# Optimization experiments

Measured on AMD Instinct MI355X. Metric: run time of the kernel, lower is better.

## Reference

```python
import jax, jax.numpy as jnp
import numpy as np

K = 3  # number_layers

def setup_inputs() -> dict:
    key = jax.random.key(0)
    k1, k2, k3, k4 = jax.random.split(key, 4)
    N, F_in, F_out, E, D = 100000, 256, 64, 1600000, 8
    x = jax.random.normal(k1, (N, F_in), dtype=jnp.float32)
    edge_attr = jax.random.uniform(k2, (E, D), dtype=jnp.float32)
    W = jax.random.normal(k3, (F_in, F_out), dtype=jnp.float32) / np.sqrt(F_in)
    b = jnp.zeros((F_out,), dtype=jnp.float32)
    edge_index = jax.random.randint(k4, (2, E), 0, N, dtype=jnp.int64)
    return {"x": x, "edge_attr": edge_attr, "W": W, "b": b, "edge_index": edge_index}

def reference(x, edge_attr, W, b, edge_index):
    N = x.shape[0]
    # edge_weight from edge_attr
    w = edge_attr.mean(axis=1)  # [E]
    src, dst = edge_index[0], edge_index[1]
    # gcn_norm: add self-loops with weight 1, symmetric normalization
    loop = jnp.arange(N, dtype=edge_index.dtype)
    src_f = jnp.concatenate([src, loop])
    dst_f = jnp.concatenate([dst, loop])
    w_f = jnp.concatenate([w, jnp.ones((N,), dtype=x.dtype)])
    deg = jax.ops.segment_sum(w_f, dst_f, num_segments=N)  # in-degree
    dinv = jnp.where(deg > 0, jax.lax.rsqrt(deg), 0.0)
    norm = dinv[src_f] * w_f * dinv[dst_f]  # [E+N]
    # K hops of x <- A_hat x
    h = x
    for _ in range(K):
        msg = norm[:, None] * h[src_f]              # gather [E+N, F]
        h = jax.ops.segment_sum(msg, dst_f, num_segments=N)  # scatter-add
    out = h @ W + b
    out = jax.nn.relu(out)
    # dropout is a no-op in eval mode
    return jax.nn.log_softmax(out, axis=-1)
```

## Files before the change

kernel.cpp:

```cpp
#include <hip/hip_runtime.h>
#include <hip/hip_bf16.h>


#define F_IN 256
#define F_OUT 64


__global__ __launch_bounds__(256) void init_kernel(float* __restrict__ deg, int* __restrict__ cnt, int N) {
    int i = blockIdx.x * 256 + threadIdx.x;
    if (i < N) { deg[i] = 1.0f; cnt[i] = 0; }
}

__global__ __launch_bounds__(256) void edgew_kernel(const float* __restrict__ ea,
                                                    const int* __restrict__ ei,
                                                    int E, int N, float* __restrict__ w,
                                                    float* __restrict__ deg, int* __restrict__ cnt) {
    int e = blockIdx.x * 256 + threadIdx.x;
    if (e >= E) return;
    const float4* a = (const float4*)(ea + (size_t)e * 8);
    float4 a0 = a[0], a1 = a[1];
    float wv = (a0.x + a0.y + a0.z + a0.w + a1.x + a1.y + a1.z + a1.w) * 0.125f;
    w[e] = wv;
    int d = ei[E + e];
    if ((unsigned)d >= (unsigned)N) return;
    atomicAdd(&deg[d], wv);
    atomicAdd(&cnt[d], 1);
}

__global__ __launch_bounds__(256) void scan1_kernel(const int* __restrict__ cnt, int* __restrict__ ptr,
                                                    int* __restrict__ bsum, int N) {
    __shared__ int s[256];
    int tid = threadIdx.x;
    int base = blockIdx.x * 1024 + tid * 4;
    int c0 = (base + 0 < N) ? cnt[base + 0] : 0;
    int c1 = (base + 1 < N) ? cnt[base + 1] : 0;
    int c2 = (base + 2 < N) ? cnt[base + 2] : 0;
    int c3 = (base + 3 < N) ? cnt[base + 3] : 0;
    int tsum = c0 + c1 + c2 + c3;
    s[tid] = tsum;
    __syncthreads();
    for (int off = 1; off < 256; off <<= 1) {
        int t = (tid >= off) ? s[tid - off] : 0;
        __syncthreads();
        s[tid] += t;
        __syncthreads();
    }
    int excl = s[tid] - tsum;
    if (base + 0 < N) ptr[base + 0] = excl;
    if (base + 1 < N) ptr[base + 1] = excl + c0;
    if (base + 2 < N) ptr[base + 2] = excl + c0 + c1;
    if (base + 3 < N) ptr[base + 3] = excl + c0 + c1 + c2;
    if (tid == 255) bsum[blockIdx.x] = s[255];
}

__global__ __launch_bounds__(256) void scan2_kernel(const int* __restrict__ bsum, int* __restrict__ bscan, int nb) {
    __shared__ int s[256];
    int tid = threadIdx.x;
    int v = (tid < nb) ? bsum[tid] : 0;
    s[tid] = v;
    __syncthreads();
    for (int off = 1; off < 256; off <<= 1) {
        int t = (tid >= off) ? s[tid - off] : 0;
        __syncthreads();
        s[tid] += t;
        __syncthreads();
    }
    if (tid < nb) bscan[tid] = s[tid] - v;
}

__global__ __launch_bounds__(256) void scan3_kernel(int* __restrict__ ptr, const int* __restrict__ bscan,
                                                    int* __restrict__ cursor, float* __restrict__ deg, int N) {
    int i = blockIdx.x * 256 + threadIdx.x;
    if (i < N) {
        int p = ptr[i] + bscan[i >> 10];
        ptr[i] = p;
        cursor[i] = p;
        deg[i] = rsqrtf(deg[i]);
    }
}

__global__ __launch_bounds__(256) void fill_kernel(const int* __restrict__ ei,
                                                   const float* __restrict__ w,
                                                   const float* __restrict__ dinv,
                                                   int* __restrict__ cursor,
                                                   int2* __restrict__ csr, int E, int N) {
    int e = blockIdx.x * 256 + threadIdx.x;
    if (e >= E) return;
    int s = ei[e];
    int d = ei[E + e];
    if ((unsigned)s >= (unsigned)N || (unsigned)d >= (unsigned)N) return;
    float nrm = dinv[s] * w[e] * dinv[d];
    int slot = atomicAdd(&cursor[d], 1);
    csr[slot] = make_int2(s, __float_as_int(nrm));
}

__global__ __launch_bounds__(256) void xw_kernel(const float* __restrict__ x, const float* __restrict__ W,
                                                 float* __restrict__ y, int N) {
    __shared__ float Wl[F_IN * F_OUT];
    const float4* W4 = (const float4*)W;
    float4* Wl4 = (float4*)Wl;
    for (int i = threadIdx.x; i < F_IN * F_OUT / 4; i += 256) Wl4[i] = W4[i];
    __syncthreads();

    int wave = (blockIdx.x * 256 + threadIdx.x) >> 6;
    int nwaves = (gridDim.x * 256) >> 6;
    int lane = threadIdx.x & 63;
    int r = lane >> 4;
    int jg = lane & 15;
    int ngroups = (N + 3) >> 2;

    for (int g = wave; g < ngroups; g += nwaves) {
        int row = g * 4 + r;
        if (row >= N) continue;
        const float4* xr = (const float4*)(x + (size_t)row * F_IN);
        float ax = 0.f, ay = 0.f, az = 0.f, aw = 0.f;
#pragma unroll 4
        for (int k4 = 0; k4 < F_IN / 4; ++k4) {
            float4 xv = xr[k4];
            float4 w0 = Wl4[(k4 * 4 + 0) * 16 + jg];
            float4 w1 = Wl4[(k4 * 4 + 1) * 16 + jg];
            float4 w2 = Wl4[(k4 * 4 + 2) * 16 + jg];
            float4 w3 = Wl4[(k4 * 4 + 3) * 16 + jg];
            ax = fmaf(xv.x, w0.x, ax); ay = fmaf(xv.x, w0.y, ay); az = fmaf(xv.x, w0.z, az); aw = fmaf(xv.x, w0.w, aw);
            ax = fmaf(xv.y, w1.x, ax); ay = fmaf(xv.y, w1.y, ay); az = fmaf(xv.y, w1.z, az); aw = fmaf(xv.y, w1.w, aw);
            ax = fmaf(xv.z, w2.x, ax); ay = fmaf(xv.z, w2.y, ay); az = fmaf(xv.z, w2.z, az); aw = fmaf(xv.z, w2.w, aw);
            ax = fmaf(xv.w, w3.x, ax); ay = fmaf(xv.w, w3.y, ay); az = fmaf(xv.w, w3.z, az); aw = fmaf(xv.w, w3.w, aw);
        }
        float4 acc = {ax, ay, az, aw};
        ((float4*)(y + (size_t)row * F_OUT))[jg] = acc;
    }
}

__global__ __launch_bounds__(256) void prop_kernel(const float* __restrict__ hin, float* __restrict__ hout,
                                                   const int* __restrict__ ptr, const int* __restrict__ cnt,
                                                   const float* __restrict__ dinv,
                                                   const int2* __restrict__ csr, int N) {
    int node = blockIdx.x * 4 + (threadIdx.x >> 6);
    if (node >= N) return;
    int lane = threadIdx.x & 63;
    float di = dinv[node];
    float acc = di * di * hin[(size_t)node * 64 + lane];
    int p = ptr[node], c = cnt[node];
    int i = 0;
    for (; i + 4 <= c; i += 4) {
        int2 e0 = csr[p + i + 0];
        int2 e1 = csr[p + i + 1];
        int2 e2 = csr[p + i + 2];
        int2 e3 = csr[p + i + 3];
        float v0 = hin[(size_t)e0.x * 64 + lane];
        float v1 = hin[(size_t)e1.x * 64 + lane];
        float v2 = hin[(size_t)e2.x * 64 + lane];
        float v3 = hin[(size_t)e3.x * 64 + lane];
        acc = fmaf(__int_as_float(e0.y), v0, acc);
        acc = fmaf(__int_as_float(e1.y), v1, acc);
        acc = fmaf(__int_as_float(e2.y), v2, acc);
        acc = fmaf(__int_as_float(e3.y), v3, acc);
    }
    for (; i < c; ++i) {
        int2 e = csr[p + i];
        acc = fmaf(__int_as_float(e.y), hin[(size_t)e.x * 64 + lane], acc);
    }
    hout[(size_t)node * 64 + lane] = acc;
}

__global__ __launch_bounds__(256) void finalize_kernel(float* __restrict__ h, const float* __restrict__ b, int N) {
    int node = blockIdx.x * 4 + (threadIdx.x >> 6);
    if (node >= N) return;
    int lane = threadIdx.x & 63;
    float v = h[(size_t)node * 64 + lane] + b[lane];
    v = fmaxf(v, 0.0f);
    float m = v;
    for (int off = 32; off; off >>= 1) m = fmaxf(m, __shfl_xor(m, off, 64));
    float ex = expf(v - m);
    float s = ex;
    for (int off = 32; off; off >>= 1) s += __shfl_xor(s, off, 64);
    h[(size_t)node * 64 + lane] = (v - m) - logf(s);
}


extern "C" void kernel_launch(void* const* d_in, const int* in_sizes, int n_in,
                              void* d_out, int out_size, void* d_ws, size_t ws_size,
                              hipStream_t stream) {
    const float* x = (const float*)d_in[0];
    const float* edge_attr = (const float*)d_in[1];
    const float* W = (const float*)d_in[2];
    const float* b = (const float*)d_in[3];
    const int* ei = (const int*)d_in[4];
    int N = in_sizes[0] / F_IN;
    int E = in_sizes[4] / 2;
    float* out = (float*)d_out;

    char* ws = (char*)d_ws;
    size_t off = 0;
    auto alloc = [&](size_t bytes) -> char* {
        char* p = ws + off;
        off += (bytes + 255) & ~(size_t)255;
        return p;
    };
    float* deg    = (float*)alloc((size_t)N * 4);
    int*   cnt    = (int*)alloc((size_t)N * 4);
    int*   ptr    = (int*)alloc((size_t)N * 4);
    int*   cursor = (int*)alloc((size_t)N * 4);
    int*   bsum   = (int*)alloc(256 * 4);
    int*   bscan  = (int*)alloc(256 * 4);
    float* w      = (float*)alloc((size_t)E * 4);
    int2*  csr    = (int2*)alloc((size_t)E * 8);
    float* h0     = (float*)alloc((size_t)N * 64 * 4);

    int nbN = (N + 255) / 256;
    int nbE = (E + 255) / 256;
    int nb1024 = (N + 1023) / 1024;
    int nbNode4 = (N + 3) / 4;

    init_kernel<<<nbN, 256, 0, stream>>>(deg, cnt, N);
    edgew_kernel<<<nbE, 256, 0, stream>>>(edge_attr, ei, E, N, w, deg, cnt);
    scan1_kernel<<<nb1024, 256, 0, stream>>>(cnt, ptr, bsum, N);
    scan2_kernel<<<1, 256, 0, stream>>>(bsum, bscan, nb1024);
    scan3_kernel<<<nbN, 256, 0, stream>>>(ptr, bscan, cursor, deg, N);
    fill_kernel<<<nbE, 256, 0, stream>>>(ei, w, deg, cursor, csr, E, N);

    xw_kernel<<<1024, 256, 0, stream>>>(x, W, h0, N);

    prop_kernel<<<nbNode4, 256, 0, stream>>>(h0, out, ptr, cnt, deg, csr, N);
    prop_kernel<<<nbNode4, 256, 0, stream>>>(out, h0, ptr, cnt, deg, csr, N);
    prop_kernel<<<nbNode4, 256, 0, stream>>>(h0, out, ptr, cnt, deg, csr, N);

    finalize_kernel<<<nbNode4, 256, 0, stream>>>(out, b, N);
}
```

Baseline: 733.7 us.

## Factor symmetric normalization out of edges; compute degree from CSR instead of atomics

Drops the float atomicAdd on degree in the edge kernel. Degree is now computed per node by summing the raw edge weights stored in CSR, which is deterministic. The edges keep the raw weight, and the D^-1/2 scaling is moved onto node features: the input is pre-scaled by dinv after XW, each hop scales by dinv^2, and finalize rescales by sqrt(deg). This removes contended float atomics and the per-edge dinv gathers, at the cost of an extra pass over the CSR and slightly different float rounding.

```diff
diff --git a/kernel.cpp b/kernel.cpp
--- a/kernel.cpp
+++ b/kernel.cpp
@@ -6,15 +6,15 @@
 #define F_OUT 64
 
 
-__global__ __launch_bounds__(256) void init_kernel(float* __restrict__ deg, int* __restrict__ cnt, int N) {
+__global__ __launch_bounds__(256) void init_kernel(int* __restrict__ cnt, int N) {
     int i = blockIdx.x * 256 + threadIdx.x;
-    if (i < N) { deg[i] = 1.0f; cnt[i] = 0; }
+    if (i < N) cnt[i] = 0;
 }
 
 __global__ __launch_bounds__(256) void edgew_kernel(const float* __restrict__ ea,
                                                     const int* __restrict__ ei,
                                                     int E, int N, float* __restrict__ w,
-                                                    float* __restrict__ deg, int* __restrict__ cnt) {
+                                                    int* __restrict__ cnt) {
     int e = blockIdx.x * 256 + threadIdx.x;
     if (e >= E) return;
     const float4* a = (const float4*)(ea + (size_t)e * 8);
@@ -23,7 +23,6 @@
     w[e] = wv;
     int d = ei[E + e];
     if ((unsigned)d >= (unsigned)N) return;
-    atomicAdd(&deg[d], wv);
     atomicAdd(&cnt[d], 1);
 }
 
@@ -69,19 +68,17 @@
 }
 
 __global__ __launch_bounds__(256) void scan3_kernel(int* __restrict__ ptr, const int* __restrict__ bscan,
-                                                    int* __restrict__ cursor, float* __restrict__ deg, int N) {
+                                                    int* __restrict__ cursor, int N) {
     int i = blockIdx.x * 256 + threadIdx.x;
     if (i < N) {
         int p = ptr[i] + bscan[i >> 10];
         ptr[i] = p;
         cursor[i] = p;
-        deg[i] = rsqrtf(deg[i]);
     }
 }
 
 __global__ __launch_bounds__(256) void fill_kernel(const int* __restrict__ ei,
                                                    const float* __restrict__ w,
-                                                   const float* __restrict__ dinv,
                                                    int* __restrict__ cursor,
                                                    int2* __restrict__ csr, int E, int N) {
     int e = blockIdx.x * 256 + threadIdx.x;
@@ -89,12 +86,24 @@
     int s = ei[e];
     int d = ei[E + e];
     if ((unsigned)s >= (unsigned)N || (unsigned)d >= (unsigned)N) return;
-    float nrm = dinv[s] * w[e] * dinv[d];
     int slot = atomicAdd(&cursor[d], 1);
-    csr[slot] = make_int2(s, __float_as_int(nrm));
+    csr[slot] = make_int2(s, __float_as_int(w[e]));
+}
+
+__global__ __launch_bounds__(256) void degk_kernel(const int* __restrict__ ptr, const int* __restrict__ cnt,
+                                                   const int2* __restrict__ csr,
+                                                   float* __restrict__ dinv, float* __restrict__ sqrtdeg, int N) {
+    int i = blockIdx.x * 256 + threadIdx.x;
+    if (i >= N) return;
+    int p = ptr[i], c = cnt[i];
+    float deg = 1.0f;
+    for (int j = 0; j < c; ++j) deg += __int_as_float(csr[p + j].y);
+    dinv[i] = rsqrtf(deg);
+    sqrtdeg[i] = sqrtf(deg);
 }
 
 __global__ __launch_bounds__(256) void xw_kernel(const float* __restrict__ x, const float* __restrict__ W,
+                                                 const float* __restrict__ dinv,
                                                  float* __restrict__ y, int N) {
     __shared__ float Wl[F_IN * F_OUT];
     const float4* W4 = (const float4*)W;
@@ -126,20 +135,20 @@
             ax = fmaf(xv.z, w2.x, ax); ay = fmaf(xv.z, w2.y, ay); az = fmaf(xv.z, w2.z, az); aw = fmaf(xv.z, w2.w, aw);
             ax = fmaf(xv.w, w3.x, ax); ay = fmaf(xv.w, w3.y, ay); az = fmaf(xv.w, w3.z, az); aw = fmaf(xv.w, w3.w, aw);
         }
-        float4 acc = {ax, ay, az, aw};
+        float di = dinv[row];
+        float4 acc = {ax * di, ay * di, az * di, aw * di};
         ((float4*)(y + (size_t)row * F_OUT))[jg] = acc;
     }
 }
 
-__global__ __launch_bounds__(256) void prop_kernel(const float* __restrict__ hin, float* __restrict__ hout,
+__global__ __launch_bounds__(256) void prop_kernel(const float* __restrict__ gin, float* __restrict__ gout,
                                                    const int* __restrict__ ptr, const int* __restrict__ cnt,
                                                    const float* __restrict__ dinv,
                                                    const int2* __restrict__ csr, int N) {
     int node = blockIdx.x * 4 + (threadIdx.x >> 6);
     if (node >= N) return;
     int lane = threadIdx.x & 63;
-    float di = dinv[node];
-    float acc = di * di * hin[(size_t)node * 64 + lane];
+    float acc = gin[(size_t)node * 64 + lane];
     int p = ptr[node], c = cnt[node];
     int i = 0;
     for (; i + 4 <= c; i += 4) {
@@ -147,10 +156,10 @@
         int2 e1 = csr[p + i + 1];
         int2 e2 = csr[p + i + 2];
         int2 e3 = csr[p + i + 3];
-        float v0 = hin[(size_t)e0.x * 64 + lane];
-        float v1 = hin[(size_t)e1.x * 64 + lane];
-        float v2 = hin[(size_t)e2.x * 64 + lane];
-        float v3 = hin[(size_t)e3.x * 64 + lane];
+        float v0 = gin[(size_t)e0.x * 64 + lane];
+        float v1 = gin[(size_t)e1.x * 64 + lane];
+        float v2 = gin[(size_t)e2.x * 64 + lane];
+        float v3 = gin[(size_t)e3.x * 64 + lane];
         acc = fmaf(__int_as_float(e0.y), v0, acc);
         acc = fmaf(__int_as_float(e1.y), v1, acc);
         acc = fmaf(__int_as_float(e2.y), v2, acc);
@@ -158,16 +167,18 @@
     }
     for (; i < c; ++i) {
         int2 e = csr[p + i];
-        acc = fmaf(__int_as_float(e.y), hin[(size_t)e.x * 64 + lane], acc);
-    }
-    hout[(size_t)node * 64 + lane] = acc;
-}
-
-__global__ __launch_bounds__(256) void finalize_kernel(float* __restrict__ h, const float* __restrict__ b, int N) {
+        acc = fmaf(__int_as_float(e.y), gin[(size_t)e.x * 64 + lane], acc);
+    }
+    float di = dinv[node];
+    gout[(size_t)node * 64 + lane] = acc * di * di;
+}
+
+__global__ __launch_bounds__(256) void finalize_kernel(float* __restrict__ h, const float* __restrict__ b,
+                                                       const float* __restrict__ sqrtdeg, int N) {
     int node = blockIdx.x * 4 + (threadIdx.x >> 6);
     if (node >= N) return;
     int lane = threadIdx.x & 63;
-    float v = h[(size_t)node * 64 + lane] + b[lane];
+    float v = h[(size_t)node * 64 + lane] * sqrtdeg[node] + b[lane];
     v = fmaxf(v, 0.0f);
     float m = v;
     for (int off = 32; off; off >>= 1) m = fmaxf(m, __shfl_xor(m, off, 64));
@@ -197,33 +208,35 @@
         off += (bytes + 255) & ~(size_t)255;
         return p;
     };
-    float* deg    = (float*)alloc((size_t)N * 4);
-    int*   cnt    = (int*)alloc((size_t)N * 4);
-    int*   ptr    = (int*)alloc((size_t)N * 4);
-    int*   cursor = (int*)alloc((size_t)N * 4);
-    int*   bsum   = (int*)alloc(256 * 4);
-    int*   bscan  = (int*)alloc(256 * 4);
-    float* w      = (float*)alloc((size_t)E * 4);
-    int2*  csr    = (int2*)alloc((size_t)E * 8);
-    float* h0     = (float*)alloc((size_t)N * 64 * 4);
+    float* dinv    = (float*)alloc((size_t)N * 4);
+    float* sqrtdeg = (float*)alloc((size_t)N * 4);
+    int*   cnt     = (int*)alloc((size_t)N * 4);
+    int*   ptr     = (int*)alloc((size_t)N * 4);
+    int*   cursor  = (int*)alloc((size_t)N * 4);
+    int*   bsum    = (int*)alloc(256 * 4);
+    int*   bscan   = (int*)alloc(256 * 4);
+    float* w       = (float*)alloc((size_t)E * 4);
+    int2*  csr     = (int2*)alloc((size_t)E * 8);
+    float* h0      = (float*)alloc((size_t)N * 64 * 4);
 
     int nbN = (N + 255) / 256;
     int nbE = (E + 255) / 256;
     int nb1024 = (N + 1023) / 1024;
     int nbNode4 = (N + 3) / 4;
 
-    init_kernel<<<nbN, 256, 0, stream>>>(deg, cnt, N);
-    edgew_kernel<<<nbE, 256, 0, stream>>>(edge_attr, ei, E, N, w, deg, cnt);
+    init_kernel<<<nbN, 256, 0, stream>>>(cnt, N);
+    edgew_kernel<<<nbE, 256, 0, stream>>>(edge_attr, ei, E, N, w, cnt);
     scan1_kernel<<<nb1024, 256, 0, stream>>>(cnt, ptr, bsum, N);
     scan2_kernel<<<1, 256, 0, stream>>>(bsum, bscan, nb1024);
-    scan3_kernel<<<nbN, 256, 0, stream>>>(ptr, bscan, cursor, deg, N);
-    fill_kernel<<<nbE, 256, 0, stream>>>(ei, w, deg, cursor, csr, E, N);
-
-    xw_kernel<<<1024, 256, 0, stream>>>(x, W, h0, N);
-
-    prop_kernel<<<nbNode4, 256, 0, stream>>>(h0, out, ptr, cnt, deg, csr, N);
-    prop_kernel<<<nbNode4, 256, 0, stream>>>(out, h0, ptr, cnt, deg, csr, N);
-    prop_kernel<<<nbNode4, 256, 0, stream>>>(h0, out, ptr, cnt, deg, csr, N);
-
-    finalize_kernel<<<nbNode4, 256, 0, stream>>>(out, b, N);
-}
+    scan3_kernel<<<nbN, 256, 0, stream>>>(ptr, bscan, cursor, N);
+    fill_kernel<<<nbE, 256, 0, stream>>>(ei, w, cursor, csr, E, N);
+    degk_kernel<<<nbN, 256, 0, stream>>>(ptr, cnt, csr, dinv, sqrtdeg, N);
+
+    xw_kernel<<<1024, 256, 0, stream>>>(x, W, dinv, h0, N);
+
+    prop_kernel<<<nbNode4, 256, 0, stream>>>(h0, out, ptr, cnt, dinv, csr, N);
+    prop_kernel<<<nbNode4, 256, 0, stream>>>(out, h0, ptr, cnt, dinv, csr, N);
+    prop_kernel<<<nbNode4, 256, 0, stream>>>(h0, out, ptr, cnt, dinv, csr, N);
+
+    finalize_kernel<<<nbNode4, 256, 0, stream>>>(out, b, sqrtdeg, N);
+}
```

Result: no change. 727.6 us (-0.8%).
